# Optimization experiments

Hardware: AMD Instinct MI355X
Metric: run time of the kernel (lower is better)

## Reference

```python
import jax, jax.numpy as jnp
import numpy as np

NONLIN = jnp.tanh  # configurable gate/candidate nonlinearity ('nonlin' init arg)

T, B, I, H = 1024, 64, 256, 512


def setup_inputs() -> dict:
    key = jax.random.key(0)
    k1, k2, k3 = jax.random.split(key, 3)
    s_i = 1.0 / np.sqrt(I)
    s_h = 1.0 / np.sqrt(H)
    return {
        "x": jax.random.normal(k1, (T, B, I), dtype=jnp.float32),
        "Wi": jax.random.normal(k2, (I, 4 * H), dtype=jnp.float32) * s_i,
        "Wh": jax.random.normal(k3, (H, 4 * H), dtype=jnp.float32) * s_h,
        "bi": jnp.zeros((4 * H,), dtype=jnp.float32),
        "bh": jnp.zeros((4 * H,), dtype=jnp.float32),
        "h0": jnp.zeros((B, H), dtype=jnp.float32),
        "c0": jnp.zeros((B, H), dtype=jnp.float32),
    }


def reference(x, Wi, Wh, bi, bh, h0, c0):
    # Precompute input projection for all timesteps in one big GEMM: [T,B,4H]
    x_proj = jnp.einsum('tbi,ig->tbg', x, Wi) + bi

    def step(carry, xp_t):
        h, c = carry
        gates = xp_t + h @ Wh + bh            # [B, 4H]
        i_g, f_g, g_g, o_g = jnp.split(gates, 4, axis=-1)
        i_g = jax.nn.sigmoid(i_g)
        f_g = jax.nn.sigmoid(f_g)
        o_g = jax.nn.sigmoid(o_g)
        g_g = NONLIN(g_g)
        c_new = f_g * c + i_g * g_g
        h_new = o_g * NONLIN(c_new)
        return (h_new, c_new), h_new

    (h_T, c_T), hs = jax.lax.scan(step, (h0, c0), x_proj)
    return hs  # [T, B, H] hidden states for every timestep
```

## Files before the change

kernel.cpp:

```cpp
#include <hip/hip_runtime.h>
#include <math.h>


#define TT      1024
#define BB      64
#define II      256
#define HH      512
#define G4H     2048
#define RPB     16
#define NRG     4
#define NCG     64
#define THREADS 512

typedef short  bf16x8 __attribute__((ext_vector_type(8)));
typedef float  f32x4  __attribute__((ext_vector_type(4)));

__device__ __forceinline__ unsigned int cvtpk_bf16(float a, float b) {
    unsigned int r;
    asm volatile("v_cvt_pk_bf16_f32 %0, %1, %2" : "=v"(r) : "v"(a), "v"(b));
    return r;
}

__device__ __forceinline__ void coh_load4_f4(const float* p0, const float* p1,
                                             const float* p2, const float* p3,
                                             float4& a, float4& b,
                                             float4& c, float4& d) {
    asm volatile(
        "global_load_dwordx4 %0, %4, off sc0 sc1\n\t"
        "global_load_dwordx4 %1, %5, off sc0 sc1\n\t"
        "global_load_dwordx4 %2, %6, off sc0 sc1\n\t"
        "global_load_dwordx4 %3, %7, off sc0 sc1\n\t"
        "s_waitcnt vmcnt(0)"
        : "=&v"(a), "=&v"(b), "=&v"(c), "=&v"(d)
        : "v"(p0), "v"(p1), "v"(p2), "v"(p3)
        : "memory");
}
__device__ __forceinline__ void coh_store_f(float* p, float v) {
    asm volatile("global_store_dword %0, %1, off sc0 sc1"
                 :: "v"(p), "v"(v) : "memory");
}
__device__ __forceinline__ float fast_tanh(float v) {
    const float e = __expf(-2.0f * fabsf(v));
    const float r = (1.0f - e) / (1.0f + e);
    return v < 0.0f ? -r : r;
}
__device__ __forceinline__ float sigm(float v) {
    return 1.0f / (1.0f + __expf(-v));
}

__device__ __forceinline__ void cvt_frag(float4 v0, float4 v1,
                                         uint4& hi, uint4& lo) {
    hi.x = cvtpk_bf16(v0.x, v0.y);
    hi.y = cvtpk_bf16(v0.z, v0.w);
    hi.z = cvtpk_bf16(v1.x, v1.y);
    hi.w = cvtpk_bf16(v1.z, v1.w);
    lo.x = cvtpk_bf16(v0.x - __uint_as_float(hi.x << 16),
                      v0.y - __uint_as_float(hi.x & 0xffff0000u));
    lo.y = cvtpk_bf16(v0.z - __uint_as_float(hi.y << 16),
                      v0.w - __uint_as_float(hi.y & 0xffff0000u));
    lo.z = cvtpk_bf16(v1.x - __uint_as_float(hi.z << 16),
                      v1.y - __uint_as_float(hi.z & 0xffff0000u));
    lo.w = cvtpk_bf16(v1.z - __uint_as_float(hi.w << 16),
                      v1.w - __uint_as_float(hi.w & 0xffff0000u));
}

__global__ void init_ctr(unsigned int* ctr) { ctr[threadIdx.x] = 0; }

__global__ __launch_bounds__(THREADS) void lstm_persist(
    const float* __restrict__ x,
    const float* __restrict__ Wi,
    const float* __restrict__ Wh,
    const float* __restrict__ bi,
    const float* __restrict__ bh,
    const float* __restrict__ h0p,
    const float* __restrict__ c0p,
    float* __restrict__ out,
    unsigned int* __restrict__ ctr)
{
    const int tid   = threadIdx.x;
    const int cg    = blockIdx.x & 63;
    const int rg    = blockIdx.x >> 6;
    const int row0  = rg * RPB;
    const int cell0 = cg * 8;
    const int wv    = tid >> 6;
    const int lane  = tid & 63;
    const int n2    = wv >> 2;
    const int k4    = wv & 3;

    __shared__ uint4 aFH[24 * 64];
    __shared__ uint4 aFL[24 * 64];
    __shared__ float red[8 * 64 * 4];
    __shared__ float c_lds[RPB][8];

    const int s_ls = tid & 63;
    const int s_r  = s_ls & 15;
    const int s_kb = (tid >> 6) * 32 + ((s_ls >> 4) & 3) * 8;

    bf16x8 wH[6], wL[6];
    {
        const int col = n2 * 16 + (lane & 15);
        const int J   = (col >> 3) * HH + cell0 + (col & 7);
        #pragma unroll
        for (int s = 0; s < 6; ++s) {
            const int kk = (s < 2) ? (k4 * 2 + s) : (8 + k4 * 4 + (s - 2));
            const int kb = kk * 32 + (lane >> 4) * 8;
            float w[8];
            #pragma unroll
            for (int e = 0; e < 8; ++e) {
                const int k = kb + e;
                w[e] = (k < II) ? Wi[(size_t)k * G4H + J]
                                : Wh[(size_t)(k - II) * G4H + J];
            }
            uint4 hi, lo;
            cvt_frag(make_float4(w[0], w[1], w[2], w[3]),
                     make_float4(w[4], w[5], w[6], w[7]), hi, lo);
            wH[s] = *(bf16x8*)&hi;
            wL[s] = *(bf16x8*)&lo;
        }
    }

    float b4[4];
    if (tid < 128) {
        const int r = tid >> 3, m8 = tid & 7;
        #pragma unroll
        for (int g = 0; g < 4; ++g)
            b4[g] = bi[g * HH + cell0 + m8] + bh[g * HH + cell0 + m8];
        c_lds[r][m8] = c0p[(size_t)(row0 + r) * HH + cell0 + m8];
    }

    {
        const float* xr = x + (size_t)(row0 + s_r) * II + s_kb;
        uint4 hi, lo;
        cvt_frag(*(const float4*)xr, *(const float4*)(xr + 4), hi, lo);
        aFH[tid] = hi; aFL[tid] = lo;

        const float* hr = h0p + (size_t)(row0 + s_r) * HH + s_kb;
        cvt_frag(*(const float4*)hr, *(const float4*)(hr + 4), hi, lo);
        aFH[512 + tid] = hi; aFL[512 + tid] = lo;
        cvt_frag(*(const float4*)(hr + 256), *(const float4*)(hr + 260), hi, lo);
        aFH[1024 + tid] = hi; aFL[1024 + tid] = lo;
    }
    __syncthreads();

    f32x4 acc = {0.f, 0.f, 0.f, 0.f};
    #pragma unroll
    for (int q = 0; q < 2; ++q) {
        const int kk = k4 * 2 + q;
        const bf16x8 ah = *(const bf16x8*)&aFH[kk * 64 + lane];
        const bf16x8 al = *(const bf16x8*)&aFL[kk * 64 + lane];
        acc = __builtin_amdgcn_mfma_f32_16x16x32_bf16(ah, wH[q], acc, 0, 0, 0);
        acc = __builtin_amdgcn_mfma_f32_16x16x32_bf16(ah, wL[q], acc, 0, 0, 0);
        acc = __builtin_amdgcn_mfma_f32_16x16x32_bf16(al, wH[q], acc, 0, 0, 0);
    }

    unsigned int* myctr = ctr + rg * 32;

    for (int t = 0; t < TT; ++t) {
        const bool more = (t + 1 < TT);

        float4 xv0, xv1;
        if (more) {
            const float* xr = x + ((size_t)(t + 1) * BB + row0 + s_r) * II + s_kb;
            xv0 = *(const float4*)xr;
            xv1 = *(const float4*)(xr + 4);
        }

        #pragma unroll
        for (int q = 0; q < 4; ++q) {
            const int kk = 8 + k4 * 4 + q;
            const bf16x8 ah = *(const bf16x8*)&aFH[kk * 64 + lane];
            const bf16x8 al = *(const bf16x8*)&aFL[kk * 64 + lane];
            acc = __builtin_amdgcn_mfma_f32_16x16x32_bf16(ah, wH[2 + q], acc, 0, 0, 0);
            acc = __builtin_amdgcn_mfma_f32_16x16x32_bf16(ah, wL[2 + q], acc, 0, 0, 0);
            acc = __builtin_amdgcn_mfma_f32_16x16x32_bf16(al, wH[2 + q], acc, 0, 0, 0);
        }

        ((f32x4*)red)[wv * 64 + lane] = acc;
        if (more) {
            uint4 hi, lo;
            cvt_frag(xv0, xv1, hi, lo);
            aFH[tid] = hi; aFL[tid] = lo;
        }
        __syncthreads();

        if (tid < 128) {
            const int r = tid >> 3, m8 = tid & 7;
            const int lane_c_base = 16 * (r >> 2);
            const int reg = r & 3;
            float g4[4];
            #pragma unroll
            for (int g = 0; g < 4; ++g) {
                const int col = g * 8 + m8;
                const int nn  = col >> 4, cl = col & 15;
                const int lc  = cl + lane_c_base;
                float s = b4[g];
                #pragma unroll
                for (int p = 0; p < 4; ++p)
                    s += red[((nn * 4 + p) * 64 + lc) * 4 + reg];
                g4[g] = s;
            }
            const float ig = sigm(g4[0]);
            const float fg = sigm(g4[1]);
            const float gg = fast_tanh(g4[2]);
            const float og = sigm(g4[3]);
            const float cn = fg * c_lds[r][m8] + ig * gg;
            c_lds[r][m8] = cn;
            coh_store_f(out + ((size_t)t * BB + row0 + r) * HH + cell0 + m8,
                        og * fast_tanh(cn));
        }

        asm volatile("s_waitcnt vmcnt(0) lgkmcnt(0)" ::: "memory");
        __syncthreads();
        if (more) {
            if (tid == 0)
                __hip_atomic_fetch_add(myctr, 1u, __ATOMIC_RELAXED,
                                       __HIP_MEMORY_SCOPE_AGENT);

            acc = (f32x4){0.f, 0.f, 0.f, 0.f};
            #pragma unroll
            for (int q = 0; q < 2; ++q) {
                const int kk = k4 * 2 + q;
                const bf16x8 ah = *(const bf16x8*)&aFH[kk * 64 + lane];
                const bf16x8 al = *(const bf16x8*)&aFL[kk * 64 + lane];
                acc = __builtin_amdgcn_mfma_f32_16x16x32_bf16(ah, wH[q], acc, 0, 0, 0);
                acc = __builtin_amdgcn_mfma_f32_16x16x32_bf16(ah, wL[q], acc, 0, 0, 0);
                acc = __builtin_amdgcn_mfma_f32_16x16x32_bf16(al, wH[q], acc, 0, 0, 0);
            }

            if (tid == 0) {
                const unsigned int target = 64u * (unsigned int)(t + 1);
                while (__hip_atomic_load(myctr, __ATOMIC_RELAXED,
                                         __HIP_MEMORY_SCOPE_AGENT) < target) {
                    __builtin_amdgcn_s_sleep(2);
                }
            }
            __syncthreads();

            {
                const float* hr = out + (size_t)t * BB * HH
                                  + (size_t)(row0 + s_r) * HH + s_kb;
                float4 v0, v1, v2, v3;
                coh_load4_f4(hr, hr + 4, hr + 256, hr + 260, v0, v1, v2, v3);
                uint4 hi, lo;
                cvt_frag(v0, v1, hi, lo);
                aFH[512 + tid] = hi; aFL[512 + tid] = lo;
                cvt_frag(v2, v3, hi, lo);
                aFH[1024 + tid] = hi; aFL[1024 + tid] = lo;
            }
            __syncthreads();
        }
    }
}

extern "C" void kernel_launch(void* const* d_in, const int* in_sizes, int n_in,
                              void* d_out, int out_size, void* d_ws, size_t ws_size,
                              hipStream_t stream) {
    const float* x  = (const float*)d_in[0];
    const float* Wi = (const float*)d_in[1];
    const float* Wh = (const float*)d_in[2];
    const float* bi = (const float*)d_in[3];
    const float* bh = (const float*)d_in[4];
    const float* h0 = (const float*)d_in[5];
    const float* c0 = (const float*)d_in[6];
    float* out = (float*)d_out;
    unsigned int* ctr = (unsigned int*)d_ws;

    init_ctr<<<1, 256, 0, stream>>>(ctr);

    void* args[] = { (void*)&x, (void*)&Wi, (void*)&Wh, (void*)&bi,
                     (void*)&bh, (void*)&h0, (void*)&c0, (void*)&out,
                     (void*)&ctr };
    hipError_t e = hipLaunchCooperativeKernel((const void*)lstm_persist,
                                              dim3(NRG * NCG), dim3(THREADS),
                                              args, 0, stream);
    if (e != hipSuccess) {
        (void)hipGetLastError();
        lstm_persist<<<dim3(NRG * NCG), dim3(THREADS), 0, stream>>>(
            x, Wi, Wh, bi, bh, h0, c0, out, ctr);
    }
}
```

Baseline: 4.105 ms.

## Exchange hidden state as packed bf16 hi/lo and overlap x-projection MFMAs

Each block now writes its new hidden values into a double-buffered workspace as packed bf16 hi/lo pairs. Consumers load those and only unpack bits, instead of reading fp32 back from the output and running the split conversion. Only the two waves that do the coherent store now wait on memory before the barrier. Waves 2-7 start the next step's input-projection MFMAs before the gate-update phase instead of after the barrier. The spin-wait sleep is also shortened; together these shorten the serial critical path per timestep, at the cost of extra workspace traffic and more intricate wave roles.

```diff
diff --git a/kernel.cpp b/kernel.cpp
--- a/kernel.cpp
+++ b/kernel.cpp
@@ -20,22 +20,7 @@
     asm volatile("v_cvt_pk_bf16_f32 %0, %1, %2" : "=v"(r) : "v"(a), "v"(b));
     return r;
 }
-
-__device__ __forceinline__ void coh_load4_f4(const float* p0, const float* p1,
-                                             const float* p2, const float* p3,
-                                             float4& a, float4& b,
-                                             float4& c, float4& d) {
-    asm volatile(
-        "global_load_dwordx4 %0, %4, off sc0 sc1\n\t"
-        "global_load_dwordx4 %1, %5, off sc0 sc1\n\t"
-        "global_load_dwordx4 %2, %6, off sc0 sc1\n\t"
-        "global_load_dwordx4 %3, %7, off sc0 sc1\n\t"
-        "s_waitcnt vmcnt(0)"
-        : "=&v"(a), "=&v"(b), "=&v"(c), "=&v"(d)
-        : "v"(p0), "v"(p1), "v"(p2), "v"(p3)
-        : "memory");
-}
-__device__ __forceinline__ void coh_store_f(float* p, float v) {
+__device__ __forceinline__ void coh_store_u(unsigned int* p, unsigned int v) {
     asm volatile("global_store_dword %0, %1, off sc0 sc1"
                  :: "v"(p), "v"(v) : "memory");
 }
@@ -64,7 +49,20 @@
                       v1.w - __uint_as_float(hi.w & 0xffff0000u));
 }
 
-__global__ void init_ctr(unsigned int* ctr) { ctr[threadIdx.x] = 0; }
+__device__ __forceinline__ void unpack8(uint4 a, uint4 b,
+                                        uint4& fh, uint4& fl) {
+    fh.x = (a.x >> 16) | (a.y & 0xffff0000u);
+    fh.y = (a.z >> 16) | (a.w & 0xffff0000u);
+    fh.z = (b.x >> 16) | (b.y & 0xffff0000u);
+    fh.w = (b.z >> 16) | (b.w & 0xffff0000u);
+    fl.x = (a.x & 0xffffu) | (a.y << 16);
+    fl.y = (a.z & 0xffffu) | (a.w << 16);
+    fl.z = (b.x & 0xffffu) | (b.w == 0 && false ? 0u : (b.w << 16));
+    fl.z = (b.x & 0xffffu) | (b.y << 16);
+    fl.w = (b.z & 0xffffu) | (b.w << 16);
+}
+
+__global__ void init_ctr(unsigned int* c) { c[threadIdx.x] = 0; }
 
 __global__ __launch_bounds__(THREADS) void lstm_persist(
     const float* __restrict__ x,
@@ -75,6 +73,7 @@
     const float* __restrict__ h0p,
     const float* __restrict__ c0p,
     float* __restrict__ out,
+    unsigned int* __restrict__ hpk,
     unsigned int* __restrict__ ctr)
 {
     const int tid   = threadIdx.x;
@@ -182,6 +181,19 @@
             aFH[tid] = hi; aFL[tid] = lo;
         }
         __syncthreads();
+
+        if (more && wv >= 2) {
+            acc = (f32x4){0.f, 0.f, 0.f, 0.f};
+            #pragma unroll
+            for (int q = 0; q < 2; ++q) {
+                const int kk = k4 * 2 + q;
+                const bf16x8 ah = *(const bf16x8*)&aFH[kk * 64 + lane];
+                const bf16x8 al = *(const bf16x8*)&aFL[kk * 64 + lane];
+                acc = __builtin_amdgcn_mfma_f32_16x16x32_bf16(ah, wH[q], acc, 0, 0, 0);
+                acc = __builtin_amdgcn_mfma_f32_16x16x32_bf16(ah, wL[q], acc, 0, 0, 0);
+                acc = __builtin_amdgcn_mfma_f32_16x16x32_bf16(al, wH[q], acc, 0, 0, 0);
+            }
+        }
 
         if (tid < 128) {
             const int r = tid >> 3, m8 = tid & 7;
@@ -205,47 +217,64 @@
             const float og = sigm(g4[3]);
             const float cn = fg * c_lds[r][m8] + ig * gg;
             c_lds[r][m8] = cn;
-            coh_store_f(out + ((size_t)t * BB + row0 + r) * HH + cell0 + m8,
-                        og * fast_tanh(cn));
-        }
-
-        asm volatile("s_waitcnt vmcnt(0) lgkmcnt(0)" ::: "memory");
+            const float hv = og * fast_tanh(cn);
+            out[((size_t)t * BB + row0 + r) * HH + cell0 + m8] = hv;
+            if (more) {
+                const unsigned int hb = cvtpk_bf16(hv, hv) & 0xffffu;
+                const float hf = __uint_as_float(hb << 16);
+                const unsigned int lb = cvtpk_bf16(hv - hf, hv - hf) & 0xffffu;
+                coh_store_u(&hpk[((size_t)(t & 1) * BB + row0 + r) * HH
+                                 + cell0 + m8], (hb << 16) | lb);
+            }
+        }
+
+        if (wv < 2) asm volatile("s_waitcnt vmcnt(0) lgkmcnt(0)" ::: "memory");
         __syncthreads();
         if (more) {
             if (tid == 0)
                 __hip_atomic_fetch_add(myctr, 1u, __ATOMIC_RELAXED,
                                        __HIP_MEMORY_SCOPE_AGENT);
 
-            acc = (f32x4){0.f, 0.f, 0.f, 0.f};
-            #pragma unroll
-            for (int q = 0; q < 2; ++q) {
-                const int kk = k4 * 2 + q;
-                const bf16x8 ah = *(const bf16x8*)&aFH[kk * 64 + lane];
-                const bf16x8 al = *(const bf16x8*)&aFL[kk * 64 + lane];
-                acc = __builtin_amdgcn_mfma_f32_16x16x32_bf16(ah, wH[q], acc, 0, 0, 0);
-                acc = __builtin_amdgcn_mfma_f32_16x16x32_bf16(ah, wL[q], acc, 0, 0, 0);
-                acc = __builtin_amdgcn_mfma_f32_16x16x32_bf16(al, wH[q], acc, 0, 0, 0);
+            if (wv < 2) {
+                acc = (f32x4){0.f, 0.f, 0.f, 0.f};
+                #pragma unroll
+                for (int q = 0; q < 2; ++q) {
+                    const int kk = k4 * 2 + q;
+                    const bf16x8 ah = *(const bf16x8*)&aFH[kk * 64 + lane];
+                    const bf16x8 al = *(const bf16x8*)&aFL[kk * 64 + lane];
+                    acc = __builtin_amdgcn_mfma_f32_16x16x32_bf16(ah, wH[q], acc, 0, 0, 0);
+                    acc = __builtin_amdgcn_mfma_f32_16x16x32_bf16(ah, wL[q], acc, 0, 0, 0);
+                    acc = __builtin_amdgcn_mfma_f32_16x16x32_bf16(al, wH[q], acc, 0, 0, 0);
+                }
             }
 
             if (tid == 0) {
                 const unsigned int target = 64u * (unsigned int)(t + 1);
                 while (__hip_atomic_load(myctr, __ATOMIC_RELAXED,
                                          __HIP_MEMORY_SCOPE_AGENT) < target) {
-                    __builtin_amdgcn_s_sleep(2);
+                    __builtin_amdgcn_s_sleep(1);
                 }
             }
             __syncthreads();
 
+            const unsigned int* hb = hpk + ((size_t)(t & 1) * BB + row0 + s_r) * HH + s_kb;
+            uint4 q0, q1, q2, q3;
+            asm volatile(
+                "global_load_dwordx4 %0, %4, off sc0 sc1\n\t"
+                "global_load_dwordx4 %1, %4, off offset:16 sc0 sc1\n\t"
+                "global_load_dwordx4 %2, %4, off offset:1024 sc0 sc1\n\t"
+                "global_load_dwordx4 %3, %4, off offset:1040 sc0 sc1\n\t"
+                "s_waitcnt vmcnt(0)"
+                : "=&v"(q0), "=&v"(q1), "=&v"(q2), "=&v"(q3)
+                : "v"(hb)
+                : "memory");
+
             {
-                const float* hr = out + (size_t)t * BB * HH
-                                  + (size_t)(row0 + s_r) * HH + s_kb;
-                float4 v0, v1, v2, v3;
-                coh_load4_f4(hr, hr + 4, hr + 256, hr + 260, v0, v1, v2, v3);
-                uint4 hi, lo;
-                cvt_frag(v0, v1, hi, lo);
-                aFH[512 + tid] = hi; aFL[512 + tid] = lo;
-                cvt_frag(v2, v3, hi, lo);
-                aFH[1024 + tid] = hi; aFL[1024 + tid] = lo;
+                uint4 fh, fl;
+                unpack8(q0, q1, fh, fl);
+                aFH[512 + tid] = fh; aFL[512 + tid] = fl;
+                unpack8(q2, q3, fh, fl);
+                aFH[1024 + tid] = fh; aFL[1024 + tid] = fl;
             }
             __syncthreads();
         }
@@ -263,19 +292,21 @@
     const float* h0 = (const float*)d_in[5];
     const float* c0 = (const float*)d_in[6];
     float* out = (float*)d_out;
-    unsigned int* ctr = (unsigned int*)d_ws;
-
-    init_ctr<<<1, 256, 0, stream>>>(ctr);
+
+    unsigned int* hpk = (unsigned int*)d_ws;
+    unsigned int* ctr = (unsigned int*)((char*)d_ws + 2 * BB * HH * 4);
+
+    init_ctr<<<1, 128, 0, stream>>>(ctr);
 
     void* args[] = { (void*)&x, (void*)&Wi, (void*)&Wh, (void*)&bi,
                      (void*)&bh, (void*)&h0, (void*)&c0, (void*)&out,
-                     (void*)&ctr };
+                     (void*)&hpk, (void*)&ctr };
     hipError_t e = hipLaunchCooperativeKernel((const void*)lstm_persist,
                                               dim3(NRG * NCG), dim3(THREADS),
                                               args, 0, stream);
     if (e != hipSuccess) {
         (void)hipGetLastError();
         lstm_persist<<<dim3(NRG * NCG), dim3(THREADS), 0, stream>>>(
-            x, Wi, Wh, bi, bh, h0, c0, out, ctr);
-    }
-}
+            x, Wi, Wh, bi, bh, h0, c0, out, hpk, ctr);
+    }
+}
```

Result: slower. 4.294 ms (+4.6%).
